# Kernel optimization log

Measured on AMD Instinct MI355X. Metric: run time of the kernel, lower is better.

The kernel has to match this reference:

```python
import jax, jax.numpy as jnp
import numpy as np

B, T_PLUS_2, H, K = 128, 2050, 64, 100
BETA = 1.0


def setup_inputs() -> dict:
    key = jax.random.key(0)
    ks = jax.random.split(key, 7)
    event_tensor = jax.random.randint(ks[0], (B, T_PLUS_2), 0, K)            # fine event types
    dtime_tensor = jax.random.uniform(ks[1], (B, T_PLUS_2), dtype=jnp.float32)
    scale = 1.0 / np.sqrt(H)
    in_emb = jax.random.normal(ks[2], (K + 3, H), dtype=jnp.float32) * scale  # +BOS/EOS/PAD rows
    Wx = jax.random.normal(ks[3], (H, 7 * H), dtype=jnp.float32) * scale      # input -> 7 gates
    Wh = jax.random.normal(ks[4], (H, 7 * H), dtype=jnp.float32) * scale      # hidden -> 7 gates
    b = jnp.zeros((7 * H,), dtype=jnp.float32)
    out_emb = jax.random.normal(ks[5], (K, H), dtype=jnp.float32) * scale     # coarse-type embeddings
    return {"event_tensor": event_tensor, "dtime_tensor": dtime_tensor,
            "in_emb": in_emb, "Wx": Wx, "Wh": Wh, "b": b, "out_emb": out_emb}


def _ctlstm_intensities(event_tensor, dtime_tensor, in_emb, Wx, Wh, b, out_emb):
    # Embed input events for steps 0..T (drop last token): [B, T+1, H]
    emb = in_emb[event_tensor[:, :-1]]
    # Precompute the input-dependent part of all 7 gates outside the scan.
    pre = jnp.einsum('bth,hg->btg', emb, Wx) + b        # [B, T+1, 7H]
    dt = dtime_tensor[:, 1:]                            # [B, T+1] dtime to next event

    batch = event_tensor.shape[0]
    h_dim = in_emb.shape[1]
    init = (jnp.zeros((batch, h_dim), jnp.float32),     # c(t_i-)
            jnp.zeros((batch, h_dim), jnp.float32),     # cell_bar
            jnp.zeros((batch, h_dim), jnp.float32))     # h(t_i-)

    def step(carry, inp):
        c_minus, cb_prev, h_minus = carry
        pre_t, dt_t = inp                               # [B,7H], [B]
        g = pre_t + h_minus @ Wh
        gi, gf, gz, go, gib, gfb, gd = jnp.split(g, 7, axis=-1)
        i = jax.nn.sigmoid(gi)
        f = jax.nn.sigmoid(gf)
        z = jnp.tanh(gz)
        o = jax.nn.sigmoid(go)
        i_bar = jax.nn.sigmoid(gib)
        f_bar = jax.nn.sigmoid(gfb)
        delta = jax.nn.softplus(gd)
        c_i = f * c_minus + i * z
        cb_i = f_bar * cb_prev + i_bar * z
        # decay over the interval dt: c(t)=cb+(c-cb)exp(-delta dt), h=o*tanh(c)
        c_next = cb_i + (c_i - cb_i) * jnp.exp(-delta * dt_t[:, None])
        h_next = o * jnp.tanh(c_next)
        return (c_next, cb_i, h_next), h_next

    _, hs = jax.lax.scan(step, init, (pre.transpose(1, 0, 2), dt.T))
    hs = hs.transpose(1, 0, 2)                          # [B, T+1, H] hidden at t_{i+1}^-
    # softplus with beta: (1/beta) * softplus(beta * x); identity fine<->coarse map
    logits = jnp.einsum('bth,kh->btk', hs, out_emb)
    return jax.nn.softplus(BETA * logits) / BETA        # [B, T+1, K]


def reference(event_tensor, dtime_tensor, in_emb, Wx, Wh, b, out_emb):
    return _ctlstm_intensities(event_tensor, dtime_tensor, in_emb, Wx, Wh, b, out_emb)
```

## Files before the change

### kernel.cpp

```cpp
#include <hip/hip_runtime.h>
#include <math.h>

#define BB 128
#define T2 2050
#define TT 2049
#define HH 64
#define GG 448
#define KK 100
#define NE 103
#define WIN 32

#define LOG2E 1.44269504088896340736f
#define LN2   0.69314718055994530942f

__device__ __forceinline__ float frcp(float x) { return __builtin_amdgcn_rcpf(x); }

__device__ __forceinline__ float sigmoid_fast(float x) {
    return frcp(1.f + exp2f(-x * LOG2E));
}
__device__ __forceinline__ float tanh_fast(float x) {
    float e = exp2f(x * (2.f * LOG2E));
    return 1.f - 2.f * frcp(1.f + e);
}
__device__ __forceinline__ float softplus_fast(float x) {
    float t = exp2f(-fabsf(x) * LOG2E);
    return fmaxf(x, 0.f) + LN2 * log2f(1.f + t);
}
__device__ __forceinline__ float expn_fast(float x) {
    return exp2f(x * LOG2E);
}

__global__ void pre_emb_kernel(const float* __restrict__ in_emb,
                               const float* __restrict__ Wx,
                               const float* __restrict__ bias,
                               float* __restrict__ pre_emb) {
    int e = blockIdx.x;
    int t = threadIdx.x;
    float acc = bias[t];
#pragma unroll
    for (int k = 0; k < HH; ++k)
        acc = fmaf(in_emb[e * HH + k], Wx[k * GG + t], acc);
    pre_emb[e * GG + t] = acc;
}

__device__ __forceinline__ float dot64(const float* __restrict__ hs,
                                       const float* __restrict__ w) {
    const float4* h4 = (const float4*)hs;
    float a0 = 0.f, a1 = 0.f, a2 = 0.f, a3 = 0.f;
#pragma unroll
    for (int k4 = 0; k4 < HH / 4; ++k4) {
        float4 hv = h4[k4];
        a0 = fmaf(hv.x, w[4 * k4 + 0], a0);
        a1 = fmaf(hv.y, w[4 * k4 + 1], a1);
        a2 = fmaf(hv.z, w[4 * k4 + 2], a2);
        a3 = fmaf(hv.w, w[4 * k4 + 3], a3);
    }
    return (a0 + a1) + (a2 + a3);
}

__launch_bounds__(576, 1)
__global__ void scan_kernel(const int* __restrict__ event,
                            const float* __restrict__ dtime,
                            const float* __restrict__ pre_emb,
                            const float* __restrict__ Wh,
                            const float* __restrict__ out_emb,
                            float* __restrict__ out) {
    const int b   = blockIdx.x;
    const int tid = threadIdx.x;
    const int w   = tid >> 6;

    __shared__ __align__(16) float h_s[HH];
    __shared__ float gbuf[GG];
    __shared__ float obuf[WIN * KK];

    const bool is_mat = tid < GG;
    const int  r      = tid - GG;
    const bool is_log = (tid >= GG) && (r < KK);

    float wcol[HH];
    if (is_mat) {
#pragma unroll
        for (int k = 0; k < HH; ++k) wcol[k] = Wh[k * GG + tid];
    } else if (is_log) {
#pragma unroll
        for (int k = 0; k < HH; ++k) wcol[k] = out_emb[r * HH + k];
    }

    if (tid < HH) h_s[tid] = 0.f;
    float c = 0.f, cb = 0.f;

    const int*   ev_row  = event + b * T2;
    const float* dt_row  = dtime + b * T2;
    float*       out_row = out + (size_t)b * TT * KK;

    float pe_cur = 0.f;
    int   evn    = 0;
    if (is_mat) {
        int ev0 = ev_row[0];
        pe_cur  = pre_emb[ev0 * GG + tid];
        evn     = ev_row[1];
    }
    float dtc = 0.f;
    if (tid < HH) dtc = dt_row[1];

    __syncthreads();

    for (int t = 0; t < TT; ++t) {
        float pe_nxt = 0.f, dtn = 0.f;
        const int tn = (t + 2 < T2) ? (t + 2) : (T2 - 1);
        if (is_mat) {
            pe_nxt = pre_emb[evn * GG + tid];
            evn    = ev_row[tn];
            if (tid < HH) dtn = dt_row[tn];

            float acc = pe_cur + dot64(h_s, wcol);
            float val;
            if (w == 2)      val = tanh_fast(acc);
            else if (w == 6) val = softplus_fast(acc);
            else             val = sigmoid_fast(acc);
            gbuf[tid] = val;
        } else {
            if (t >= WIN + 1 && ((t - 1) & (WIN - 1)) == 0) {
                const int base = t - 1 - WIN;
                const int i = tid - GG;
#pragma unroll
                for (int j = 0; j < (WIN * KK) / 128; ++j) {
                    const int idx = j * 128 + i;
                    out_row[(size_t)base * KK + idx] = obuf[idx];
                }
            }
            if (is_log && t >= 1) {
                float lg = dot64(h_s, wcol);
                obuf[((t - 1) & (WIN - 1)) * KK + r] = softplus_fast(lg);
            }
        }
        __syncthreads();
        if (tid < HH) {
            const float gi  = gbuf[tid];
            const float gf  = gbuf[HH + tid];
            const float gz  = gbuf[2 * HH + tid];
            const float go  = gbuf[3 * HH + tid];
            const float gib = gbuf[4 * HH + tid];
            const float gfb = gbuf[5 * HH + tid];
            const float gd  = gbuf[6 * HH + tid];
            const float ci  = fmaf(gf, c, gi * gz);
            const float cbi = fmaf(gfb, cb, gib * gz);
            const float cn  = fmaf(ci - cbi, expn_fast(-gd * dtc), cbi);
            const float h   = go * tanh_fast(cn);
            c   = cn;
            cb  = cbi;
            dtc = dtn;
            h_s[tid] = h;
        }
        if (is_mat) pe_cur = pe_nxt;
        __syncthreads();
    }

    if (tid >= GG) {
        const int base = ((TT - 1) / WIN) * WIN - 0;
        const int fbase = TT - 1 - WIN;
        const int i = tid - GG;
#pragma unroll
        for (int j = 0; j < (WIN * KK) / 128; ++j) {
            const int idx = j * 128 + i;
            out_row[(size_t)fbase * KK + idx] = obuf[idx];
        }
        (void)base;
        if (r < KK) {
            float lg = dot64(h_s, wcol);
            out_row[(size_t)(TT - 1) * KK + r] = softplus_fast(lg);
        }
    }
}

extern "C" void kernel_launch(void* const* d_in, const int* in_sizes, int n_in,
                              void* d_out, int out_size, void* d_ws, size_t ws_size,
                              hipStream_t stream) {
    const int*   event  = (const int*)d_in[0];
    const float* dtime  = (const float*)d_in[1];
    const float* in_emb = (const float*)d_in[2];
    const float* Wx     = (const float*)d_in[3];
    const float* Wh     = (const float*)d_in[4];
    const float* bias   = (const float*)d_in[5];
    const float* oe     = (const float*)d_in[6];
    float*       out    = (float*)d_out;

    float* pre_emb = (float*)d_ws;

    pre_emb_kernel<<<NE, GG, 0, stream>>>(in_emb, Wx, bias, pre_emb);
    scan_kernel<<<BB, 576, 0, stream>>>(event, dtime, pre_emb, Wh, oe, out);
}
```

Baseline: 1.632 ms.

## Split logits into separate kernel and compute cell update redundantly per wave

The scan kernel drops its output-logit threads and runs with 448 threads. Each of the 7 waves now recomputes the 64-wide cell/hidden update redundantly into its own shared copy of h, which removes one barrier per timestep. Gate values are double-buffered, and exp(-softplus*dt) is folded into the gate stage. Hidden states are staged in the output buffer, and a second, fully parallel kernel reads them back to compute the softplus logits in place. This trades extra global traffic and a second launch for a shorter serial critical path.

```diff
diff --git a/kernel.cpp b/kernel.cpp
--- a/kernel.cpp
+++ b/kernel.cpp
@@ -8,7 +8,8 @@
 #define GG 448
 #define KK 100
 #define NE 103
-#define WIN 32
+#define TCHUNK 128
+#define NCHUNK 17
 
 #define LOG2E 1.44269504088896340736f
 #define LN2   0.69314718055994530942f
@@ -58,117 +59,121 @@
     return (a0 + a1) + (a2 + a3);
 }
 
-__launch_bounds__(576, 1)
+__launch_bounds__(GG, 1)
 __global__ void scan_kernel(const int* __restrict__ event,
                             const float* __restrict__ dtime,
                             const float* __restrict__ pre_emb,
                             const float* __restrict__ Wh,
-                            const float* __restrict__ out_emb,
                             float* __restrict__ out) {
-    const int b   = blockIdx.x;
-    const int tid = threadIdx.x;
-    const int w   = tid >> 6;
+    const int b    = blockIdx.x;
+    const int tid  = threadIdx.x;
+    const int w    = tid >> 6;
+    const int lane = tid & 63;
 
-    __shared__ __align__(16) float h_s[HH];
-    __shared__ float gbuf[GG];
-    __shared__ float obuf[WIN * KK];
-
-    const bool is_mat = tid < GG;
-    const int  r      = tid - GG;
-    const bool is_log = (tid >= GG) && (r < KK);
+    __shared__ __align__(16) float gbuf[2][GG];
+    __shared__ __align__(16) float h_sw[7][HH];
 
     float wcol[HH];
-    if (is_mat) {
 #pragma unroll
-        for (int k = 0; k < HH; ++k) wcol[k] = Wh[k * GG + tid];
-    } else if (is_log) {
-#pragma unroll
-        for (int k = 0; k < HH; ++k) wcol[k] = out_emb[r * HH + k];
-    }
-
-    if (tid < HH) h_s[tid] = 0.f;
-    float c = 0.f, cb = 0.f;
+    for (int k = 0; k < HH; ++k) wcol[k] = Wh[k * GG + tid];
 
     const int*   ev_row  = event + b * T2;
     const float* dt_row  = dtime + b * T2;
     float*       out_row = out + (size_t)b * TT * KK;
 
-    float pe_cur = 0.f;
-    int   evn    = 0;
-    if (is_mat) {
-        int ev0 = ev_row[0];
-        pe_cur  = pre_emb[ev0 * GG + tid];
-        evn     = ev_row[1];
+    {
+        int   ev0 = ev_row[0];
+        float pe0 = pre_emb[ev0 * GG + tid];
+        float dt0 = dt_row[1];
+        float v0;
+        if (w == 2)      v0 = tanh_fast(pe0);
+        else if (w == 6) v0 = expn_fast(-softplus_fast(pe0) * dt0);
+        else             v0 = sigmoid_fast(pe0);
+        gbuf[0][tid] = v0;
     }
-    float dtc = 0.f;
-    if (tid < HH) dtc = dt_row[1];
 
+    float pe_cur = pre_emb[ev_row[1] * GG + tid];
+    int   evn    = ev_row[2];
+    float dt_cur = dt_row[2];
+
+    float c = 0.f, cb = 0.f;
     __syncthreads();
 
     for (int t = 0; t < TT; ++t) {
-        float pe_nxt = 0.f, dtn = 0.f;
-        const int tn = (t + 2 < T2) ? (t + 2) : (T2 - 1);
-        if (is_mat) {
+        const bool more = (t < TT - 1);
+        float pe_nxt = 0.f, dt_new = 0.f;
+        int   ev_new = 0;
+        if (more) {
             pe_nxt = pre_emb[evn * GG + tid];
-            evn    = ev_row[tn];
-            if (tid < HH) dtn = dt_row[tn];
+            int tn = (t + 3 < T2) ? (t + 3) : (T2 - 1);
+            ev_new = ev_row[tn];
+            dt_new = dt_row[tn];
+        }
 
-            float acc = pe_cur + dot64(h_s, wcol);
+        const float* gb = gbuf[t & 1];
+        const float gi  = gb[lane];
+        const float gf  = gb[HH + lane];
+        const float gz  = gb[2 * HH + lane];
+        const float go  = gb[3 * HH + lane];
+        const float gib = gb[4 * HH + lane];
+        const float gfb = gb[5 * HH + lane];
+        const float ed  = gb[6 * HH + lane];
+        const float ci  = fmaf(gf, c, gi * gz);
+        const float cbi = fmaf(gfb, cb, gib * gz);
+        const float cn  = fmaf(ci - cbi, ed, cbi);
+        const float h   = go * tanh_fast(cn);
+        c  = cn;
+        cb = cbi;
+
+        if (tid < HH) out_row[(size_t)t * KK + tid] = h;
+
+        h_sw[w][lane] = h;
+
+        if (more) {
+            float acc = pe_cur + dot64(h_sw[w], wcol);
             float val;
             if (w == 2)      val = tanh_fast(acc);
-            else if (w == 6) val = softplus_fast(acc);
+            else if (w == 6) val = expn_fast(-softplus_fast(acc) * dt_cur);
             else             val = sigmoid_fast(acc);
-            gbuf[tid] = val;
-        } else {
-            if (t >= WIN + 1 && ((t - 1) & (WIN - 1)) == 0) {
-                const int base = t - 1 - WIN;
-                const int i = tid - GG;
-#pragma unroll
-                for (int j = 0; j < (WIN * KK) / 128; ++j) {
-                    const int idx = j * 128 + i;
-                    out_row[(size_t)base * KK + idx] = obuf[idx];
-                }
-            }
-            if (is_log && t >= 1) {
-                float lg = dot64(h_s, wcol);
-                obuf[((t - 1) & (WIN - 1)) * KK + r] = softplus_fast(lg);
-            }
+            gbuf[(t + 1) & 1][tid] = val;
+            pe_cur = pe_nxt;
+            evn    = ev_new;
+            dt_cur = dt_new;
         }
         __syncthreads();
-        if (tid < HH) {
-            const float gi  = gbuf[tid];
-            const float gf  = gbuf[HH + tid];
-            const float gz  = gbuf[2 * HH + tid];
-            const float go  = gbuf[3 * HH + tid];
-            const float gib = gbuf[4 * HH + tid];
-            const float gfb = gbuf[5 * HH + tid];
-            const float gd  = gbuf[6 * HH + tid];
-            const float ci  = fmaf(gf, c, gi * gz);
-            const float cbi = fmaf(gfb, cb, gib * gz);
-            const float cn  = fmaf(ci - cbi, expn_fast(-gd * dtc), cbi);
-            const float h   = go * tanh_fast(cn);
-            c   = cn;
-            cb  = cbi;
-            dtc = dtn;
-            h_s[tid] = h;
-        }
-        if (is_mat) pe_cur = pe_nxt;
-        __syncthreads();
+    }
+}
+
+__launch_bounds__(128)
+__global__ void logits_kernel(const float* __restrict__ oe,
+                              float* __restrict__ out) {
+    const int b   = blockIdx.x;
+    const int t0  = blockIdx.y * TCHUNK;
+    const int nt  = (TT - t0 < TCHUNK) ? (TT - t0) : TCHUNK;
+    const int tid = threadIdx.x;
+
+    __shared__ __align__(16) float hs[TCHUNK][HH];
+
+    float* row = out + ((size_t)b * TT + t0) * KK;
+
+    const int n4 = nt * (HH / 4);
+    for (int i4 = tid; i4 < n4; i4 += 128) {
+        int tt = i4 >> 4, q = i4 & 15;
+        ((float4*)&hs[tt][0])[q] = ((const float4*)(row + (size_t)tt * KK))[q];
     }
 
-    if (tid >= GG) {
-        const int base = ((TT - 1) / WIN) * WIN - 0;
-        const int fbase = TT - 1 - WIN;
-        const int i = tid - GG;
+    float wk[HH];
+    if (tid < KK) {
 #pragma unroll
-        for (int j = 0; j < (WIN * KK) / 128; ++j) {
-            const int idx = j * 128 + i;
-            out_row[(size_t)fbase * KK + idx] = obuf[idx];
-        }
-        (void)base;
-        if (r < KK) {
-            float lg = dot64(h_s, wcol);
-            out_row[(size_t)(TT - 1) * KK + r] = softplus_fast(lg);
+        for (int q = 0; q < HH / 4; ++q)
+            ((float4*)wk)[q] = ((const float4*)(oe + tid * HH))[q];
+    }
+    __syncthreads();
+
+    if (tid < KK) {
+        for (int tt = 0; tt < nt; ++tt) {
+            float lg = dot64(&hs[tt][0], wk);
+            row[(size_t)tt * KK + tid] = softplus_fast(lg);
         }
     }
 }
@@ -188,5 +193,6 @@
     float* pre_emb = (float*)d_ws;
 
     pre_emb_kernel<<<NE, GG, 0, stream>>>(in_emb, Wx, bias, pre_emb);
-    scan_kernel<<<BB, 576, 0, stream>>>(event, dtime, pre_emb, Wh, oe, out);
+    scan_kernel<<<BB, GG, 0, stream>>>(event, dtime, pre_emb, Wh, out);
+    logits_kernel<<<dim3(BB, NCHUNK), 128, 0, stream>>>(oe, out);
 }
```

Result: no change. 1.661 ms (+1.8%).

## Restructure LSTM scan with redundant per-wave cell update and single barrier per step

Applied to the files above, without the earlier changes.

Each of the 7 gate waves now redundantly computes the cell/hidden update for all 64 units from a double-buffered gate array, writes h to its own LDS copy, and then computes its gate matvec. This removes one of the two block barriers per timestep. The decay exp(-delta*dt) is folded into the softplus gate evaluation. Each thread now handles two columns over half of K, with a cross-half shuffle reduction. Events and dtimes are staged into LDS up front, the logit waves write outputs directly instead of through a windowed buffer, and gate waves get raised scheduling priority. The cost is redundant per-wave cell math and a more intricate pipelined ordering that is easy to get wrong.

```diff
diff --git a/kernel.cpp b/kernel.cpp
--- a/kernel.cpp
+++ b/kernel.cpp
@@ -8,7 +8,8 @@
 #define GG 448
 #define KK 100
 #define NE 103
-#define WIN 32
+#define NSTAGE 2056
+#define NTHREADS 576
 
 #define LOG2E 1.44269504088896340736f
 #define LN2   0.69314718055994530942f
@@ -25,9 +26,6 @@
 __device__ __forceinline__ float softplus_fast(float x) {
     float t = exp2f(-fabsf(x) * LOG2E);
     return fmaxf(x, 0.f) + LN2 * log2f(1.f + t);
-}
-__device__ __forceinline__ float expn_fast(float x) {
-    return exp2f(x * LOG2E);
 }
 
 __global__ void pre_emb_kernel(const float* __restrict__ in_emb,
@@ -43,134 +41,185 @@
     pre_emb[e * GG + t] = acc;
 }
 
-__device__ __forceinline__ float dot64(const float* __restrict__ hs,
-                                       const float* __restrict__ w) {
-    const float4* h4 = (const float4*)hs;
-    float a0 = 0.f, a1 = 0.f, a2 = 0.f, a3 = 0.f;
-#pragma unroll
-    for (int k4 = 0; k4 < HH / 4; ++k4) {
-        float4 hv = h4[k4];
-        a0 = fmaf(hv.x, w[4 * k4 + 0], a0);
-        a1 = fmaf(hv.y, w[4 * k4 + 1], a1);
-        a2 = fmaf(hv.z, w[4 * k4 + 2], a2);
-        a3 = fmaf(hv.w, w[4 * k4 + 3], a3);
-    }
-    return (a0 + a1) + (a2 + a3);
-}
-
-__launch_bounds__(576, 1)
+__device__ __forceinline__ void step_barrier() {
+    __builtin_amdgcn_sched_barrier(0);
+    asm volatile("s_waitcnt lgkmcnt(0)" ::: "memory");
+    __builtin_amdgcn_s_barrier();
+    __builtin_amdgcn_sched_barrier(0);
+}
+
+__launch_bounds__(NTHREADS, 1)
 __global__ void scan_kernel(const int* __restrict__ event,
                             const float* __restrict__ dtime,
                             const float* __restrict__ pre_emb,
                             const float* __restrict__ Wh,
-                            const float* __restrict__ out_emb,
+                            const float* __restrict__ oe,
                             float* __restrict__ out) {
     const int b   = blockIdx.x;
     const int tid = threadIdx.x;
     const int w   = tid >> 6;
-
-    __shared__ __align__(16) float h_s[HH];
-    __shared__ float gbuf[GG];
-    __shared__ float obuf[WIN * KK];
-
-    const bool is_mat = tid < GG;
-    const int  r      = tid - GG;
-    const bool is_log = (tid >= GG) && (r < KK);
-
-    float wcol[HH];
-    if (is_mat) {
-#pragma unroll
-        for (int k = 0; k < HH; ++k) wcol[k] = Wh[k * GG + tid];
-    } else if (is_log) {
-#pragma unroll
-        for (int k = 0; k < HH; ++k) wcol[k] = out_emb[r * HH + k];
-    }
-
-    if (tid < HH) h_s[tid] = 0.f;
-    float c = 0.f, cb = 0.f;
+    const int l   = tid & 63;
+    const int h2  = l >> 5;
+    const int s5  = l & 31;
+
+    __shared__ float gbuf[2][7][HH];
+    __shared__ __align__(16) float h_sw[7][2][HH];
+    __shared__ int   evoff_s[NSTAGE];
+    __shared__ float dtl_s[NSTAGE];
+
+    const bool is_gate = (w < 7);
+    const int  jw      = w - 7;
 
     const int*   ev_row  = event + b * T2;
     const float* dt_row  = dtime + b * T2;
     float*       out_row = out + (size_t)b * TT * KK;
 
-    float pe_cur = 0.f;
-    int   evn    = 0;
-    if (is_mat) {
-        int ev0 = ev_row[0];
-        pe_cur  = pre_emb[ev0 * GG + tid];
-        evn     = ev_row[1];
-    }
-    float dtc = 0.f;
-    if (tid < HH) dtc = dt_row[1];
+    for (int i = tid; i < NSTAGE; i += NTHREADS) {
+        const int idx = (i < T2) ? i : (T2 - 1);
+        evoff_s[i] = ev_row[idx] * GG;
+        dtl_s[i]   = dt_row[idx];
+    }
+
+    float wA[32], wB[32];
+    if (is_gate) {
+        const int cA = w * 64 + s5;
+        const int cB = w * 64 + 32 + s5;
+#pragma unroll
+        for (int kk = 0; kk < 32; ++kk) {
+            const int k = 32 * h2 + kk;
+            wA[kk] = Wh[k * GG + cA];
+            wB[kk] = Wh[k * GG + cB];
+        }
+    } else {
+        int cA = 64 * jw + s5;       if (cA > KK - 1) cA = KK - 1;
+        int cB = 64 * jw + 32 + s5;  if (cB > KK - 1) cB = KK - 1;
+#pragma unroll
+        for (int j = 0; j < 8; ++j) {
+            ((float4*)wA)[j] = ((const float4*)(oe + cA * HH + 32 * h2))[j];
+            ((float4*)wB)[j] = ((const float4*)(oe + cB * HH + 32 * h2))[j];
+        }
+    }
 
     __syncthreads();
 
-    for (int t = 0; t < TT; ++t) {
-        float pe_nxt = 0.f, dtn = 0.f;
-        const int tn = (t + 2 < T2) ? (t + 2) : (T2 - 1);
-        if (is_mat) {
-            pe_nxt = pre_emb[evn * GG + tid];
-            evn    = ev_row[tn];
-            if (tid < HH) dtn = dt_row[tn];
-
-            float acc = pe_cur + dot64(h_s, wcol);
-            float val;
-            if (w == 2)      val = tanh_fast(acc);
-            else if (w == 6) val = softplus_fast(acc);
-            else             val = sigmoid_fast(acc);
-            gbuf[tid] = val;
-        } else {
-            if (t >= WIN + 1 && ((t - 1) & (WIN - 1)) == 0) {
-                const int base = t - 1 - WIN;
-                const int i = tid - GG;
-#pragma unroll
-                for (int j = 0; j < (WIN * KK) / 128; ++j) {
-                    const int idx = j * 128 + i;
-                    out_row[(size_t)base * KK + idx] = obuf[idx];
-                }
-            }
-            if (is_log && t >= 1) {
-                float lg = dot64(h_s, wcol);
-                obuf[((t - 1) & (WIN - 1)) * KK + r] = softplus_fast(lg);
-            }
-        }
-        __syncthreads();
-        if (tid < HH) {
-            const float gi  = gbuf[tid];
-            const float gf  = gbuf[HH + tid];
-            const float gz  = gbuf[2 * HH + tid];
-            const float go  = gbuf[3 * HH + tid];
-            const float gib = gbuf[4 * HH + tid];
-            const float gfb = gbuf[5 * HH + tid];
-            const float gd  = gbuf[6 * HH + tid];
-            const float ci  = fmaf(gf, c, gi * gz);
-            const float cbi = fmaf(gfb, cb, gib * gz);
-            const float cn  = fmaf(ci - cbi, expn_fast(-gd * dtc), cbi);
-            const float h   = go * tanh_fast(cn);
-            c   = cn;
-            cb  = cbi;
-            dtc = dtn;
-            h_s[tid] = h;
-        }
-        if (is_mat) pe_cur = pe_nxt;
-        __syncthreads();
-    }
-
-    if (tid >= GG) {
-        const int base = ((TT - 1) / WIN) * WIN - 0;
-        const int fbase = TT - 1 - WIN;
-        const int i = tid - GG;
-#pragma unroll
-        for (int j = 0; j < (WIN * KK) / 128; ++j) {
-            const int idx = j * 128 + i;
-            out_row[(size_t)fbase * KK + idx] = obuf[idx];
-        }
-        (void)base;
-        if (r < KK) {
-            float lg = dot64(h_s, wcol);
-            out_row[(size_t)(TT - 1) * KK + r] = softplus_fast(lg);
-        }
-    }
+    const int colOff = w * 64 + 32 * h2 + s5;
+    float preE = 0.f, preO = 0.f, dtE = 0.f, dtO = 0.f;
+    int   offE = 0, offO = 0;
+    if (is_gate) {
+        const float p0  = pre_emb[evoff_s[0] + colOff];
+        const float dt0 = dtl_s[1];
+        float v0;
+        if (w == 2)      v0 = tanh_fast(p0);
+        else if (w == 6) v0 = exp2f(-dt0 * log2f(1.f + exp2f(p0 * LOG2E)));
+        else             v0 = sigmoid_fast(p0);
+        gbuf[0][w][32 * h2 + s5] = v0;
+
+        preE = pre_emb[evoff_s[1] + colOff];
+        preO = pre_emb[evoff_s[2] + colOff];
+        offE = evoff_s[3];
+        offO = evoff_s[4];
+        dtE  = dtl_s[2];
+        dtO  = dtl_s[3];
+    }
+    __syncthreads();
+
+    float c = 0.f, cb = 0.f;
+
+    const int  lcolA = 64 * jw + s5;
+    const int  lcolB = 64 * jw + 32 + s5;
+    float*     outP  = out_row;
+
+#define GATE_STEP(RB, WB, PRE, OFF, DTV, TIDX)                                  \
+    {                                                                           \
+        const float pre_use = PRE;                                              \
+        PRE = pre_emb[OFF + colOff];                \
+        OFF = evoff_s[(TIDX) + 5];                                              \
+        const float dt_use = DTV;                                               \
+        DTV = dtl_s[(TIDX) + 4];                                                \
+                \
+        const float g0 = gbuf[RB][0][l];                                        \
+        const float g1 = gbuf[RB][1][l];                                        \
+        const float g2 = gbuf[RB][2][l];                                        \
+        const float g3 = gbuf[RB][3][l];                                        \
+        const float g4 = gbuf[RB][4][l];                                        \
+        const float g5 = gbuf[RB][5][l];                                        \
+        const float g6 = gbuf[RB][6][l];        \
+        const float ci  = fmaf(g1, c, g0 * g2);                                 \
+        const float cbi = fmaf(g5, cb, g4 * g2);                                \
+        const float cn  = fmaf(ci - cbi, g6, cbi);                              \
+        const float h   = g3 * tanh_fast(cn);                                   \
+        c  = cn;                                                                \
+        cb = cbi;                                                               \
+        h_sw[w][RB][l] = h;                                                     \
+                     \
+        const float4* h4 = (const float4*)&h_sw[w][RB][32 * h2];                \
+        float pA = 0.f, pB = 0.f;                                               \
+        _Pragma("unroll") for (int j = 0; j < 8; ++j) {                         \
+            const float4 hv = h4[j];                                            \
+            pA = fmaf(hv.x, wA[4 * j + 0], pA);                                 \
+            pB = fmaf(hv.x, wB[4 * j + 0], pB);                                 \
+            pA = fmaf(hv.y, wA[4 * j + 1], pA);                                 \
+            pB = fmaf(hv.y, wB[4 * j + 1], pB);                                 \
+            pA = fmaf(hv.z, wA[4 * j + 2], pA);                                 \
+            pB = fmaf(hv.z, wB[4 * j + 2], pB);                                 \
+            pA = fmaf(hv.w, wA[4 * j + 3], pA);                                 \
+            pB = fmaf(hv.w, wB[4 * j + 3], pB);                                 \
+        }                                                                       \
+        pA += __shfl_xor(pA, 32);                                               \
+        pB += __shfl_xor(pB, 32);                                               \
+        const float acc = pre_use + (h2 ? pB : pA);                             \
+        float val;                                                              \
+        if (w == 2)      val = tanh_fast(acc);                                  \
+        else if (w == 6) val = exp2f(-dt_use * log2f(1.f + exp2f(acc * LOG2E)));\
+        else             val = sigmoid_fast(acc);                               \
+        gbuf[WB][w][32 * h2 + s5] = val;                                        \
+    }
+
+#define LOGIT_STEP(HB, DO_STORE)                                                \
+    {                                                                           \
+        const float4* h4 = (const float4*)&h_sw[0][HB][32 * h2];                \
+        float pA = 0.f, pB = 0.f;                                               \
+        _Pragma("unroll") for (int j = 0; j < 8; ++j) {                         \
+            const float4 hv = h4[j];                                            \
+            pA = fmaf(hv.x, wA[4 * j + 0], pA);                                 \
+            pB = fmaf(hv.x, wB[4 * j + 0], pB);                                 \
+            pA = fmaf(hv.y, wA[4 * j + 1], pA);                                 \
+            pB = fmaf(hv.y, wB[4 * j + 1], pB);                                 \
+            pA = fmaf(hv.z, wA[4 * j + 2], pA);                                 \
+            pB = fmaf(hv.z, wB[4 * j + 2], pB);                                 \
+            pA = fmaf(hv.w, wA[4 * j + 3], pA);                                 \
+            pB = fmaf(hv.w, wB[4 * j + 3], pB);                                 \
+        }                                                                       \
+        pA += __shfl_xor(pA, 32);                                               \
+        pB += __shfl_xor(pB, 32);                                               \
+        if (DO_STORE) {                                                         \
+            const float lg  = h2 ? pB : pA;                                     \
+            const int   col = h2 ? lcolB : lcolA;                               \
+            if (col < KK) outP[col] = softplus_fast(lg);                        \
+            outP += KK;                                                         \
+        }                                                                       \
+    }
+
+    if (is_gate) __builtin_amdgcn_s_setprio(1);
+
+    for (int tp = 0; tp < (TT - 1) / 2; ++tp) {
+        const int te = 2 * tp;
+        if (is_gate) { GATE_STEP(0, 1, preE, offE, dtE, te) }
+        else         { LOGIT_STEP(1, (tp > 0)) }
+        step_barrier();
+        if (is_gate) { GATE_STEP(1, 0, preO, offO, dtO, te + 1) }
+        else         { LOGIT_STEP(0, true) }
+        step_barrier();
+    }
+    if (is_gate) { GATE_STEP(0, 1, preE, offE, dtE, TT - 1) }
+    else         { LOGIT_STEP(1, true) }
+    step_barrier();
+    if (is_gate) __builtin_amdgcn_s_setprio(0);
+
+    if (!is_gate) { LOGIT_STEP(0, true) }
+
+#undef GATE_STEP
+#undef LOGIT_STEP
 }
 
 extern "C" void kernel_launch(void* const* d_in, const int* in_sizes, int n_in,
@@ -188,5 +237,5 @@
     float* pre_emb = (float*)d_ws;
 
     pre_emb_kernel<<<NE, GG, 0, stream>>>(in_emb, Wx, bias, pre_emb);
-    scan_kernel<<<BB, 576, 0, stream>>>(event, dtime, pre_emb, Wh, oe, out);
-}
+    scan_kernel<<<BB, NTHREADS, 0, stream>>>(event, dtime, pre_emb, Wh, oe, out);
+}
```

Result: faster. 1.395 ms (-14.5%).
